# Kernel tuning notes

Hardware: AMD Instinct MI355X
Metric: run time of the kernel (lower is better)

## Reference

```python
import jax, jax.numpy as jnp
import numpy as np

B, N, C, H = 8, 4096, 768, 8


def setup_inputs() -> dict:
    key = jax.random.key(0)
    k1, k2, k3 = jax.random.split(key, 3)
    x = jax.random.normal(k1, (B, N, C), dtype=jnp.float32)
    W_qkv = jax.random.normal(k2, (C, 3 * C), dtype=jnp.float32) * 0.02
    W_proj = jax.random.normal(k3, (C, C), dtype=jnp.float32) * 0.02
    b_proj = jnp.zeros((C,), dtype=jnp.float32)
    temp = jnp.ones((H, 1, 1), dtype=jnp.float32)
    return {"x": x, "W_qkv": W_qkv, "W_proj": W_proj, "b_proj": b_proj, "temp": temp}


def reference(x, W_qkv, W_proj, b_proj, temp):
    b, n, c = x.shape
    h = temp.shape[0]
    d = c // h
    # qkv: [B,N,3C] -> [B,N,H,D,3]  (matches tf.reshape split order)
    qkv = (x @ W_qkv).reshape(b, n, h, d, 3)
    q, k, v = qkv[..., 0], qkv[..., 1], qkv[..., 2]
    # L2-normalize along the patch axis (axis=1), as tf.linalg.normalize
    q = q / jnp.linalg.norm(q, axis=1, keepdims=True)
    k = k / jnp.linalg.norm(k, axis=1, keepdims=True)
    # channel-wise (cross-covariance) attention: [B,H,D,D]
    attn = jnp.einsum('bnhd,bnhe->bhde', q, k) * temp
    attn = jax.nn.softmax(attn, axis=-1)
    # apply to v and fold heads back: [B,N,C]
    y = jnp.einsum('bhde,bnhe->bnhd', attn, v).reshape(b, n, c)
    return y @ W_proj + b_proj
```

## Files before the change

kernel.cpp:

```cpp
#include <hip/hip_runtime.h>

typedef __attribute__((ext_vector_type(8))) short short8;
typedef __attribute__((ext_vector_type(4))) float f32x4;

__device__ inline unsigned short f2b(float f) {
  unsigned int u = __builtin_bit_cast(unsigned int, f);
  u = (u + 0x7FFFu + ((u >> 16) & 1u)) >> 16;
  return (unsigned short)u;
}
__device__ inline float b2f(unsigned short s) {
  unsigned int u = ((unsigned int)s) << 16;
  return __builtin_bit_cast(float, u);
}

__device__ inline void async16(const void* g, void* l) {
  __builtin_amdgcn_global_load_lds((__attribute__((address_space(1))) void*)(g),
                                   (__attribute__((address_space(3))) void*)(l), 16, 0, 0);
}

__global__ void cvt_x(const float4* __restrict__ x, ushort4* __restrict__ xb, int n4) {
  int i = blockIdx.x * blockDim.x + threadIdx.x;
  int stride = gridDim.x * blockDim.x;
  for (; i < n4; i += stride) {
    float4 v = x[i];
    ushort4 o;
    o.x = f2b(v.x); o.y = f2b(v.y); o.z = f2b(v.z); o.w = f2b(v.w);
    xb[i] = o;
  }
}

__global__ __launch_bounds__(256) void t_wqkv(const float* __restrict__ W, unsigned short* __restrict__ Wt) {
  __shared__ float tile[32][33];
  int j0 = blockIdx.x * 32, c0 = blockIdx.y * 32;
  int tx = threadIdx.x & 31, ty = threadIdx.x >> 5;
#pragma unroll
  for (int r = 0; r < 32; r += 8)
    tile[ty + r][tx] = W[(size_t)(c0 + ty + r) * 2304 + j0 + tx];
  __syncthreads();
#pragma unroll
  for (int r = 0; r < 32; r += 8) {
    int j = j0 + ty + r;
    int h = j / 288, rem = j - h * 288;
    int d = rem / 3, s = rem - d * 3;
    int jj = s * 768 + h * 96 + d;
    Wt[(size_t)jj * 768 + c0 + tx] = f2b(tile[tx][ty + r]);
  }
}

__global__ __launch_bounds__(256) void t_wproj(const float* __restrict__ W, unsigned short* __restrict__ Wt) {
  __shared__ float tile[32][33];
  int j0 = blockIdx.x * 32, c0 = blockIdx.y * 32;
  int tx = threadIdx.x & 31, ty = threadIdx.x >> 5;
#pragma unroll
  for (int r = 0; r < 32; r += 8)
    tile[ty + r][tx] = W[(size_t)(c0 + ty + r) * 768 + j0 + tx];
  __syncthreads();
#pragma unroll
  for (int r = 0; r < 32; r += 8)
    Wt[(size_t)(j0 + ty + r) * 768 + c0 + tx] = f2b(tile[tx][ty + r]);
}

__global__ __launch_bounds__(512, 2) void gemm_qkv(
    const unsigned short* __restrict__ A, const unsigned short* __restrict__ Bt,
    unsigned short* __restrict__ Q, unsigned short* __restrict__ Kd, unsigned short* __restrict__ V) {
  extern __shared__ __align__(16) unsigned short smem[];
  const int tid = threadIdx.x;
  const int wave = tid >> 6, lane = tid & 63;
  const int mlane = lane & 15, quad = lane >> 4;
  const int m0 = blockIdx.x * 256, n0 = blockIdx.y * 256;
  const int ah = wave >> 2;
  const int wm = ah * 128;
  const int wn = (wave & 3) * 64;
  const int bh = wn >> 7;
  const int bl = wn & 64;

  f32x4 acc[8][4] = {};

  auto stage = [&](int kt, int c) {
    const int k0 = kt * 64;
#pragma unroll
    for (int h = 0; h < 4; ++h) {
      const unsigned short* src = (h < 2) ? A : Bt;
      const int rbase = ((h < 2) ? m0 : n0) + (h & 1) * 128;
      unsigned short* ldsbase = smem + c * 32768 + h * 8192;
#pragma unroll
      for (int i = 0; i < 2; ++i) {
        int ebase = i * 512 + (wave << 6);
        int e = ebase + lane;
        int row = e >> 3;
        int slot = (e & 7) ^ (row & 7);
        async16(src + (size_t)(rbase + row) * 768 + k0 + slot * 8, ldsbase + ebase * 8);
      }
    }
  };

  auto rdA = [&](const unsigned short* base, int mh, int kk, int f) -> short8 {
    int r = mh * 64 + f * 16 + mlane;
    return *(const short8*)&base[r * 64 + ((kk * 32 + quad * 8) ^ ((r & 7) << 3))];
  };
  auto rdB = [&](const unsigned short* base, int kk, int j) -> short8 {
    int r = bl + j * 16 + mlane;
    return *(const short8*)&base[r * 64 + ((kk * 32 + quad * 8) ^ ((r & 7) << 3))];
  };

  stage(0, 0);
  stage(1, 1);
  asm volatile("s_waitcnt vmcnt(8)" ::: "memory");
  __builtin_amdgcn_sched_barrier(0);
  __builtin_amdgcn_s_barrier();

#pragma unroll 1
  for (int t = 0; t < 12; ++t) {
    const int c = t & 1;
    const unsigned short* Abase = smem + c * 32768 + ah * 8192;
    const unsigned short* Bbase = smem + c * 32768 + 16384 + bh * 8192;
    short8 a0[4], a1[4], b0[4], b1[4];

#pragma unroll
    for (int j = 0; j < 4; ++j) b0[j] = rdB(Bbase, 0, j);
#pragma unroll
    for (int f = 0; f < 4; ++f) a0[f] = rdA(Abase, 0, 0, f);
    asm volatile("s_waitcnt lgkmcnt(0)" ::: "memory");
    __builtin_amdgcn_sched_barrier(0);
    __builtin_amdgcn_s_setprio(1);
#pragma unroll
    for (int f = 0; f < 4; ++f)
#pragma unroll
      for (int j = 0; j < 4; ++j)
        acc[f][j] = __builtin_amdgcn_mfma_f32_16x16x32_bf16(a0[f], b0[j], acc[f][j], 0, 0, 0);
    __builtin_amdgcn_s_setprio(0);
    __builtin_amdgcn_s_barrier();

#pragma unroll
    for (int f = 0; f < 4; ++f) a1[f] = rdA(Abase, 1, 0, f);
#pragma unroll
    for (int j = 0; j < 4; ++j) b1[j] = rdB(Bbase, 1, j);
    asm volatile("s_waitcnt lgkmcnt(0)" ::: "memory");
    __builtin_amdgcn_sched_barrier(0);
    __builtin_amdgcn_s_setprio(1);
#pragma unroll
    for (int f = 0; f < 4; ++f)
#pragma unroll
      for (int j = 0; j < 4; ++j)
        acc[4 + f][j] = __builtin_amdgcn_mfma_f32_16x16x32_bf16(a1[f], b0[j], acc[4 + f][j], 0, 0, 0);
    __builtin_amdgcn_s_setprio(0);
    __builtin_amdgcn_s_barrier();

#pragma unroll
    for (int f = 0; f < 4; ++f) a0[f] = rdA(Abase, 0, 1, f);
#pragma unroll
    for (int f = 0; f < 4; ++f) a1[f] = rdA(Abase, 1, 1, f);
    asm volatile("s_waitcnt lgkmcnt(0)" ::: "memory");
    __builtin_amdgcn_sched_barrier(0);
    __builtin_amdgcn_s_setprio(1);
#pragma unroll
    for (int f = 0; f < 4; ++f)
#pragma unroll
      for (int j = 0; j < 4; ++j)
        acc[f][j] = __builtin_amdgcn_mfma_f32_16x16x32_bf16(a0[f], b1[j], acc[f][j], 0, 0, 0);
    __builtin_amdgcn_s_setprio(0);
    __builtin_amdgcn_s_barrier();

    if (t < 10) stage(t + 2, c);
    __builtin_amdgcn_s_setprio(1);
#pragma unroll
    for (int f = 0; f < 4; ++f)
#pragma unroll
      for (int j = 0; j < 4; ++j)
        acc[4 + f][j] = __builtin_amdgcn_mfma_f32_16x16x32_bf16(a1[f], b1[j], acc[4 + f][j], 0, 0, 0);
    __builtin_amdgcn_s_setprio(0);
    if (t < 10) {
      asm volatile("s_waitcnt vmcnt(8)" ::: "memory");
      __builtin_amdgcn_sched_barrier(0);
      __builtin_amdgcn_s_barrier();
    } else if (t == 10) {
      asm volatile("s_waitcnt vmcnt(0)" ::: "memory");
      __builtin_amdgcn_sched_barrier(0);
      __builtin_amdgcn_s_barrier();
    }
  }

  const int bb = m0 >> 12;
  const int nbase = (m0 & 4095) + wm + quad * 4;
  unsigned short* dstp[4];
  size_t cb[4];
#pragma unroll
  for (int j = 0; j < 4; ++j) {
    int jj = n0 + wn + j * 16 + mlane;
    int s = (jj >= 1536) ? 2 : (jj >= 768) ? 1 : 0;
    int hd = jj - s * 768;
    int h = hd / 96;
    int d = hd - h * 96;
    dstp[j] = (s == 0) ? Q : (s == 1) ? Kd : V;
    cb[j] = ((size_t)(bb * 8 + h) * 4096) * 96 + d;
  }
#pragma unroll
  for (int mf = 0; mf < 8; ++mf) {
    int n = nbase + (mf >> 2) * 64 + (mf & 3) * 16;
#pragma unroll
    for (int r = 0; r < 4; ++r) {
#pragma unroll
      for (int j = 0; j < 4; ++j)
        dstp[j][cb[j] + (size_t)(n + r) * 96] = f2b(acc[mf][j][r]);
    }
  }
}

__global__ __launch_bounds__(256) void attn_partial(
    const unsigned short* __restrict__ Q, const unsigned short* __restrict__ Kd,
    float* __restrict__ Spart, float* __restrict__ sq, float* __restrict__ sk) {
  int chunk = blockIdx.x;
  int bh = blockIdx.y;
  __shared__ __align__(16) unsigned short QT[96 * 72];
  __shared__ __align__(16) unsigned short KT[96 * 72];
  int t = threadIdx.x;
  int wave = t >> 6, lane = t & 63, mlane = lane & 15, quad = lane >> 4;
  int wrow = (wave >> 1) * 48, wcol = (wave & 1) * 48;
  f32x4 acc[3][3] = {};
  const unsigned int* qp = (const unsigned int*)(Q + (size_t)bh * 4096 * 96);
  const unsigned int* kp = (const unsigned int*)(Kd + (size_t)bh * 4096 * 96);
  int c = t % 48, rg = t / 48;
  int nbeg = chunk * 256;
  float aq0 = 0.f, aq1 = 0.f, ak0 = 0.f, ak1 = 0.f;
  for (int n0 = nbeg; n0 < nbeg + 256; n0 += 64) {
    __syncthreads();
    if (rg < 5) {
      for (int n = rg; n < 64; n += 5) {
        unsigned int qv = qp[(size_t)(n0 + n) * 48 + c];
        unsigned int kv = kp[(size_t)(n0 + n) * 48 + c];
        QT[(2 * c) * 72 + n] = (unsigned short)(qv & 0xffff);
        QT[(2 * c + 1) * 72 + n] = (unsigned short)(qv >> 16);
        KT[(2 * c) * 72 + n] = (unsigned short)(kv & 0xffff);
        KT[(2 * c + 1) * 72 + n] = (unsigned short)(kv >> 16);
        float q0 = b2f((unsigned short)(qv & 0xffff)), q1 = b2f((unsigned short)(qv >> 16));
        float k0 = b2f((unsigned short)(kv & 0xffff)), k1 = b2f((unsigned short)(kv >> 16));
        aq0 += q0 * q0; aq1 += q1 * q1; ak0 += k0 * k0; ak1 += k1 * k1;
      }
    }
    __syncthreads();
#pragma unroll
    for (int kk = 0; kk < 64; kk += 32) {
      short8 a[3], bf[3];
#pragma unroll
      for (int f = 0; f < 3; ++f)
        a[f] = *(const short8*)&QT[(wrow + f * 16 + mlane) * 72 + kk + quad * 8];
#pragma unroll
      for (int f = 0; f < 3; ++f)
        bf[f] = *(const short8*)&KT[(wcol + f * 16 + mlane) * 72 + kk + quad * 8];
#pragma unroll
      for (int i = 0; i < 3; ++i)
#pragma unroll
        for (int j = 0; j < 3; ++j)
          acc[i][j] = __builtin_amdgcn_mfma_f32_16x16x32_bf16(a[i], bf[j], acc[i][j], 0, 0, 0);
    }
  }
  if (rg < 5) {
    atomicAdd(&sq[bh * 96 + 2 * c], aq0);
    atomicAdd(&sq[bh * 96 + 2 * c + 1], aq1);
    atomicAdd(&sk[bh * 96 + 2 * c], ak0);
    atomicAdd(&sk[bh * 96 + 2 * c + 1], ak1);
  }
  float* dst = Spart + ((size_t)bh * 16 + chunk) * 9216;
#pragma unroll
  for (int i = 0; i < 3; ++i)
#pragma unroll
    for (int j = 0; j < 3; ++j)
#pragma unroll
      for (int r = 0; r < 4; ++r)
        dst[(wrow + i * 16 + quad * 4 + r) * 96 + wcol + j * 16 + mlane] = acc[i][j][r];
}

__global__ __launch_bounds__(256) void attn_finalize(
    const float* __restrict__ Spart, const float* __restrict__ sq,
    const float* __restrict__ sk, const float* __restrict__ temp,
    unsigned short* __restrict__ Pt) {
  int bh = blockIdx.x, h = bh & 7;
  __shared__ float S[9216];
  __shared__ float rk[96], rq[96];
  int t = threadIdx.x;
  const float* base = Spart + (size_t)bh * 16 * 9216;
  if (t < 96) {
    rk[t] = rsqrtf(sk[bh * 96 + t]);
    rq[t] = rsqrtf(sq[bh * 96 + t]) * temp[h];
  }
  __syncthreads();
  for (int i = t; i < 9216; i += 256) {
    float s = 0.f;
#pragma unroll
    for (int c2 = 0; c2 < 16; ++c2) s += base[(size_t)c2 * 9216 + i];
    int d = i / 96, e = i - d * 96;
    S[i] = s * rq[d] * rk[e];
  }
  __syncthreads();
  if (t < 96) {
    int d = t;
    float mx = -1e30f;
    for (int e = 0; e < 96; ++e) mx = fmaxf(mx, S[d * 96 + e]);
    float sum = 0.f;
    for (int e = 0; e < 96; ++e) {
      float v = expf(S[d * 96 + e] - mx);
      S[d * 96 + e] = v;
      sum += v;
    }
    float inv = 1.0f / sum;
    for (int e = 0; e < 96; ++e)
      Pt[(size_t)bh * 9216 + e * 96 + d] = f2b(S[d * 96 + e] * inv);
  }
}

__global__ __launch_bounds__(256) void m_pre(
    const unsigned short* __restrict__ Wtp, const unsigned short* __restrict__ Pt,
    unsigned short* __restrict__ Mt) {
  int bh = blockIdx.y;
  int b = bh >> 3, h = bh & 7;
  int m0 = blockIdx.x * 128;
  int t = threadIdx.x, wave = t >> 6, lane = t & 63, mlane = lane & 15, quad = lane >> 4;
  const unsigned short* Pb = Pt + (size_t)bh * 9216;
  f32x4 acc[2][6] = {};
#pragma unroll
  for (int kk = 0; kk < 96; kk += 32) {
    short8 a[2], bfr[6];
#pragma unroll
    for (int i = 0; i < 2; ++i)
      a[i] = *(const short8*)&Wtp[(size_t)(m0 + wave * 32 + i * 16 + mlane) * 768 + h * 96 + kk + quad * 8];
#pragma unroll
    for (int j = 0; j < 6; ++j)
      bfr[j] = *(const short8*)&Pb[(j * 16 + mlane) * 96 + kk + quad * 8];
#pragma unroll
    for (int i = 0; i < 2; ++i)
#pragma unroll
      for (int j = 0; j < 6; ++j)
        acc[i][j] = __builtin_amdgcn_mfma_f32_16x16x32_bf16(a[i], bfr[j], acc[i][j], 0, 0, 0);
  }
#pragma unroll
  for (int i = 0; i < 2; ++i) {
    int cp = m0 + wave * 32 + i * 16 + quad * 4;
#pragma unroll
    for (int j = 0; j < 6; ++j) {
      int e = j * 16 + mlane;
#pragma unroll
      for (int r = 0; r < 4; ++r)
        Mt[((size_t)b * 768 + cp + r) * 768 + h * 96 + e] = f2b(acc[i][j][r]);
    }
  }
}

__global__ __launch_bounds__(512, 2) void gemm_out(
    const unsigned short* __restrict__ V, const unsigned short* __restrict__ Mt,
    const float* __restrict__ bias, float* __restrict__ out) {
  extern __shared__ __align__(16) unsigned short smem[];
  const int tid = threadIdx.x;
  const int wave = tid >> 6, lane = tid & 63;
  const int mlane = lane & 15, quad = lane >> 4;
  const int m0 = blockIdx.x * 256, n0 = blockIdx.y * 256;
  const int bb = m0 >> 12;
  const int nloc0 = m0 & 4095;
  const int ah = wave >> 2;
  const int wm = ah * 128;
  const int wn = (wave & 3) * 64;
  const int bhf = wn >> 7;
  const int bl = wn & 64;

  f32x4 acc[8][4] = {};

  auto stage = [&](int kt, int c) {
#pragma unroll
    for (int h = 0; h < 4; ++h) {
      unsigned short* ldsbase = smem + c * 32768 + h * 8192;
#pragma unroll
      for (int i = 0; i < 2; ++i) {
        int ebase = i * 512 + (wave << 6);
        int e = ebase + lane;
        int row = e >> 3;
        int slot = (e & 7) ^ (row & 7);
        if (h < 2) {
          int kc = kt * 8 + slot;
          int hh = kc / 12;
          int e0 = (kc - hh * 12) * 8;
          int n = nloc0 + (h & 1) * 128 + row;
          async16(V + ((size_t)(bb * 8 + hh) * 4096 + n) * 96 + e0, ldsbase + ebase * 8);
        } else {
          int col = n0 + (h & 1) * 128 + row;
          async16(Mt + ((size_t)bb * 768 + col) * 768 + kt * 64 + slot * 8, ldsbase + ebase * 8);
        }
      }
    }
  };

  auto rdA = [&](const unsigned short* base, int mh, int kk, int f) -> short8 {
    int r = mh * 64 + f * 16 + mlane;
    return *(const short8*)&base[r * 64 + ((kk * 32 + quad * 8) ^ ((r & 7) << 3))];
  };
  auto rdB = [&](const unsigned short* base, int kk, int j) -> short8 {
    int r = bl + j * 16 + mlane;
    return *(const short8*)&base[r * 64 + ((kk * 32 + quad * 8) ^ ((r & 7) << 3))];
  };

  stage(0, 0);
  stage(1, 1);
  asm volatile("s_waitcnt vmcnt(8)" ::: "memory");
  __builtin_amdgcn_sched_barrier(0);
  __builtin_amdgcn_s_barrier();

#pragma unroll 1
  for (int t = 0; t < 12; ++t) {
    const int c = t & 1;
    const unsigned short* Abase = smem + c * 32768 + ah * 8192;
    const unsigned short* Bbase = smem + c * 32768 + 16384 + bhf * 8192;
    short8 a0[4], a1[4], b0[4], b1[4];

#pragma unroll
    for (int j = 0; j < 4; ++j) b0[j] = rdB(Bbase, 0, j);
#pragma unroll
    for (int f = 0; f < 4; ++f) a0[f] = rdA(Abase, 0, 0, f);
    asm volatile("s_waitcnt lgkmcnt(0)" ::: "memory");
    __builtin_amdgcn_sched_barrier(0);
    __builtin_amdgcn_s_setprio(1);
#pragma unroll
    for (int f = 0; f < 4; ++f)
#pragma unroll
      for (int j = 0; j < 4; ++j)
        acc[f][j] = __builtin_amdgcn_mfma_f32_16x16x32_bf16(a0[f], b0[j], acc[f][j], 0, 0, 0);
    __builtin_amdgcn_s_setprio(0);
    __builtin_amdgcn_s_barrier();

#pragma unroll
    for (int f = 0; f < 4; ++f) a1[f] = rdA(Abase, 1, 0, f);
#pragma unroll
    for (int j = 0; j < 4; ++j) b1[j] = rdB(Bbase, 1, j);
    asm volatile("s_waitcnt lgkmcnt(0)" ::: "memory");
    __builtin_amdgcn_sched_barrier(0);
    __builtin_amdgcn_s_setprio(1);
#pragma unroll
    for (int f = 0; f < 4; ++f)
#pragma unroll
      for (int j = 0; j < 4; ++j)
        acc[4 + f][j] = __builtin_amdgcn_mfma_f32_16x16x32_bf16(a1[f], b0[j], acc[4 + f][j], 0, 0, 0);
    __builtin_amdgcn_s_setprio(0);
    __builtin_amdgcn_s_barrier();

#pragma unroll
    for (int f = 0; f < 4; ++f) a0[f] = rdA(Abase, 0, 1, f);
#pragma unroll
    for (int f = 0; f < 4; ++f) a1[f] = rdA(Abase, 1, 1, f);
    asm volatile("s_waitcnt lgkmcnt(0)" ::: "memory");
    __builtin_amdgcn_sched_barrier(0);
    __builtin_amdgcn_s_setprio(1);
#pragma unroll
    for (int f = 0; f < 4; ++f)
#pragma unroll
      for (int j = 0; j < 4; ++j)
        acc[f][j] = __builtin_amdgcn_mfma_f32_16x16x32_bf16(a0[f], b1[j], acc[f][j], 0, 0, 0);
    __builtin_amdgcn_s_setprio(0);
    __builtin_amdgcn_s_barrier();

    if (t < 10) stage(t + 2, c);
    __builtin_amdgcn_s_setprio(1);
#pragma unroll
    for (int f = 0; f < 4; ++f)
#pragma unroll
      for (int j = 0; j < 4; ++j)
        acc[4 + f][j] = __builtin_amdgcn_mfma_f32_16x16x32_bf16(a1[f], b1[j], acc[4 + f][j], 0, 0, 0);
    __builtin_amdgcn_s_setprio(0);
    if (t < 10) {
      asm volatile("s_waitcnt vmcnt(8)" ::: "memory");
      __builtin_amdgcn_sched_barrier(0);
      __builtin_amdgcn_s_barrier();
    } else if (t == 10) {
      asm volatile("s_waitcnt vmcnt(0)" ::: "memory");
      __builtin_amdgcn_sched_barrier(0);
      __builtin_amdgcn_s_barrier();
    }
  }

#pragma unroll
  for (int j = 0; j < 4; ++j) {
    int col = n0 + wn + j * 16 + mlane;
    float bv = bias[col];
#pragma unroll
    for (int mf = 0; mf < 8; ++mf) {
      int m = m0 + wm + (mf >> 2) * 64 + (mf & 3) * 16 + quad * 4;
#pragma unroll
      for (int r = 0; r < 4; ++r)
        out[(size_t)(m + r) * 768 + col] = acc[mf][j][r] + bv;
    }
  }
}

extern "C" void kernel_launch(void* const* d_in, const int* in_sizes, int n_in,
                              void* d_out, int out_size, void* d_ws, size_t ws_size,
                              hipStream_t stream) {
  const float* x = (const float*)d_in[0];
  const float* Wqkv = (const float*)d_in[1];
  const float* Wproj = (const float*)d_in[2];
  const float* bias = (const float*)d_in[3];
  const float* temp = (const float*)d_in[4];
  float* out = (float*)d_out;

  char* ws = (char*)d_ws;
  size_t off = 0;
  auto alloc = [&](size_t bytes) -> void* {
    void* p = ws + off;
    off += (bytes + 255) & ~(size_t)255;
    return p;
  };
  unsigned short* xb = (unsigned short*)alloc(32768ull * 768 * 2);
  unsigned short* Wtq = (unsigned short*)alloc(2304ull * 768 * 2);
  unsigned short* Wtp = (unsigned short*)alloc(768ull * 768 * 2);
  unsigned short* Q = (unsigned short*)alloc(64ull * 4096 * 96 * 2);
  unsigned short* Kd = (unsigned short*)alloc(64ull * 4096 * 96 * 2);
  unsigned short* V = (unsigned short*)alloc(64ull * 4096 * 96 * 2);
  float* sq = (float*)alloc(64 * 96 * 4);
  float* sk = (float*)alloc(64 * 96 * 4);
  unsigned short* Pt = (unsigned short*)alloc(64ull * 9216 * 2);
  (void)off; (void)ws_size; (void)in_sizes; (void)n_in; (void)out_size;

  unsigned short* Mt = xb;

  float* Spart = out;

  static bool attr_set = false;
  if (!attr_set) {
    hipFuncSetAttribute((const void*)gemm_qkv, hipFuncAttributeMaxDynamicSharedMemorySize, 131072);
    hipFuncSetAttribute((const void*)gemm_out, hipFuncAttributeMaxDynamicSharedMemorySize, 131072);
    attr_set = true;
  }

  cvt_x<<<4096, 256, 0, stream>>>((const float4*)x, (ushort4*)xb, 32768 * 768 / 4);
  t_wqkv<<<dim3(72, 24), 256, 0, stream>>>(Wqkv, Wtq);
  t_wproj<<<dim3(24, 24), 256, 0, stream>>>(Wproj, Wtp);
  hipMemsetAsync(sq, 0, 64 * 96 * 4, stream);
  hipMemsetAsync(sk, 0, 64 * 96 * 4, stream);
  gemm_qkv<<<dim3(128, 9), 512, 131072, stream>>>(xb, Wtq, Q, Kd, V);
  attn_partial<<<dim3(16, 64), 256, 0, stream>>>(Q, Kd, Spart, sq, sk);
  attn_finalize<<<64, 256, 0, stream>>>(Spart, sq, sk, temp, Pt);
  m_pre<<<dim3(6, 64), 256, 0, stream>>>(Wtp, Pt, Mt);
  gemm_out<<<dim3(128, 3), 512, 131072, stream>>>(V, Mt, bias, out);
}
```

Baseline: 473.1 us.

## Store Q/K transposed from QKV GEMM and fuse norm sums into epilogue

The QKV GEMM epilogue now writes Q and K in a [bh][d][n] transposed layout with 8-byte vector stores, and computes the per-channel sum of squares there with wave shuffles and atomics. The attention-partial kernel then drops its LDS transpose staging and its norm accumulation, and loads MFMA operands straight from global memory with register double-buffering. This removes the scalar, bank-conflicting LDS transpose pass and the extra reads of Q and K. The cost is more atomics in the GEMM epilogue. Norms are now computed from fp32 accumulators rather than the bf16-rounded values.

```diff
diff --git a/kernel.cpp b/kernel.cpp
--- a/kernel.cpp
+++ b/kernel.cpp
@@ -62,7 +62,8 @@
 
 __global__ __launch_bounds__(512, 2) void gemm_qkv(
     const unsigned short* __restrict__ A, const unsigned short* __restrict__ Bt,
-    unsigned short* __restrict__ Q, unsigned short* __restrict__ Kd, unsigned short* __restrict__ V) {
+    unsigned short* __restrict__ Qt, unsigned short* __restrict__ Kt, unsigned short* __restrict__ V,
+    float* __restrict__ sq, float* __restrict__ sk) {
   extern __shared__ __align__(16) unsigned short smem[];
   const int tid = threadIdx.x;
   const int wave = tid >> 6, lane = tid & 63;
@@ -181,84 +182,90 @@
   }
 
   const int bb = m0 >> 12;
-  const int nbase = (m0 & 4095) + wm + quad * 4;
-  unsigned short* dstp[4];
-  size_t cb[4];
-#pragma unroll
-  for (int j = 0; j < 4; ++j) {
-    int jj = n0 + wn + j * 16 + mlane;
-    int s = (jj >= 1536) ? 2 : (jj >= 768) ? 1 : 0;
-    int hd = jj - s * 768;
-    int h = hd / 96;
-    int d = hd - h * 96;
-    dstp[j] = (s == 0) ? Q : (s == 1) ? Kd : V;
-    cb[j] = ((size_t)(bb * 8 + h) * 4096) * 96 + d;
-  }
-#pragma unroll
-  for (int mf = 0; mf < 8; ++mf) {
-    int n = nbase + (mf >> 2) * 64 + (mf & 3) * 16;
-#pragma unroll
-    for (int r = 0; r < 4; ++r) {
-#pragma unroll
-      for (int j = 0; j < 4; ++j)
-        dstp[j][cb[j] + (size_t)(n + r) * 96] = f2b(acc[mf][j][r]);
+  const int s = n0 / 768;
+  if (s < 2) {
+    unsigned short* dst = (s == 0) ? Qt : Kt;
+    float* ss = (s == 0) ? sq : sk;
+    const int n0s = n0 - s * 768;
+    const int mloc = (m0 & 4095) + wm;
+#pragma unroll
+    for (int j = 0; j < 4; ++j) {
+      int hd = n0s + wn + j * 16 + mlane;
+      int h = hd / 96, d = hd - h * 96;
+      size_t rowbase = ((size_t)(bb * 8 + h) * 96 + d) * 4096 + mloc;
+      float ssq = 0.f;
+#pragma unroll
+      for (int mf = 0; mf < 8; ++mf) {
+        int nl = (mf >> 2) * 64 + (mf & 3) * 16 + quad * 4;
+        ushort4 o;
+        o.x = f2b(acc[mf][j][0]); o.y = f2b(acc[mf][j][1]);
+        o.z = f2b(acc[mf][j][2]); o.w = f2b(acc[mf][j][3]);
+        *(ushort4*)(dst + rowbase + nl) = o;
+#pragma unroll
+        for (int r = 0; r < 4; ++r) ssq += acc[mf][j][r] * acc[mf][j][r];
+      }
+      ssq += __shfl_xor(ssq, 16);
+      ssq += __shfl_xor(ssq, 32);
+      if (quad == 0) atomicAdd(&ss[(bb * 8 + h) * 96 + d], ssq);
+    }
+  } else {
+    const int nbase = (m0 & 4095) + wm + quad * 4;
+    size_t cb[4];
+#pragma unroll
+    for (int j = 0; j < 4; ++j) {
+      int hd = n0 + wn + j * 16 + mlane - 1536;
+      int h = hd / 96;
+      int d = hd - h * 96;
+      cb[j] = ((size_t)(bb * 8 + h) * 4096) * 96 + d;
+    }
+#pragma unroll
+    for (int mf = 0; mf < 8; ++mf) {
+      int n = nbase + (mf >> 2) * 64 + (mf & 3) * 16;
+#pragma unroll
+      for (int r = 0; r < 4; ++r) {
+#pragma unroll
+        for (int j = 0; j < 4; ++j)
+          V[cb[j] + (size_t)(n + r) * 96] = f2b(acc[mf][j][r]);
+      }
     }
   }
 }
 
 __global__ __launch_bounds__(256) void attn_partial(
-    const unsigned short* __restrict__ Q, const unsigned short* __restrict__ Kd,
-    float* __restrict__ Spart, float* __restrict__ sq, float* __restrict__ sk) {
+    const unsigned short* __restrict__ Qt, const unsigned short* __restrict__ Kt,
+    float* __restrict__ Spart) {
   int chunk = blockIdx.x;
   int bh = blockIdx.y;
-  __shared__ __align__(16) unsigned short QT[96 * 72];
-  __shared__ __align__(16) unsigned short KT[96 * 72];
   int t = threadIdx.x;
   int wave = t >> 6, lane = t & 63, mlane = lane & 15, quad = lane >> 4;
   int wrow = (wave >> 1) * 48, wcol = (wave & 1) * 48;
+  const unsigned short* qp = Qt + (size_t)bh * 96 * 4096;
+  const unsigned short* kp = Kt + (size_t)bh * 96 * 4096;
   f32x4 acc[3][3] = {};
-  const unsigned int* qp = (const unsigned int*)(Q + (size_t)bh * 4096 * 96);
-  const unsigned int* kp = (const unsigned int*)(Kd + (size_t)bh * 4096 * 96);
-  int c = t % 48, rg = t / 48;
   int nbeg = chunk * 256;
-  float aq0 = 0.f, aq1 = 0.f, ak0 = 0.f, ak1 = 0.f;
-  for (int n0 = nbeg; n0 < nbeg + 256; n0 += 64) {
-    __syncthreads();
-    if (rg < 5) {
-      for (int n = rg; n < 64; n += 5) {
-        unsigned int qv = qp[(size_t)(n0 + n) * 48 + c];
-        unsigned int kv = kp[(size_t)(n0 + n) * 48 + c];
-        QT[(2 * c) * 72 + n] = (unsigned short)(qv & 0xffff);
-        QT[(2 * c + 1) * 72 + n] = (unsigned short)(qv >> 16);
-        KT[(2 * c) * 72 + n] = (unsigned short)(kv & 0xffff);
-        KT[(2 * c + 1) * 72 + n] = (unsigned short)(kv >> 16);
-        float q0 = b2f((unsigned short)(qv & 0xffff)), q1 = b2f((unsigned short)(qv >> 16));
-        float k0 = b2f((unsigned short)(kv & 0xffff)), k1 = b2f((unsigned short)(kv >> 16));
-        aq0 += q0 * q0; aq1 += q1 * q1; ak0 += k0 * k0; ak1 += k1 * k1;
+
+  short8 a[3], b[3], an[3], bn[3];
+#pragma unroll
+  for (int f = 0; f < 3; ++f) {
+    a[f] = *(const short8*)&qp[(size_t)(wrow + f * 16 + mlane) * 4096 + nbeg + quad * 8];
+    b[f] = *(const short8*)&kp[(size_t)(wcol + f * 16 + mlane) * 4096 + nbeg + quad * 8];
+  }
+#pragma unroll 1
+  for (int n0 = nbeg; n0 < nbeg + 256; n0 += 32) {
+    if (n0 + 32 < nbeg + 256) {
+#pragma unroll
+      for (int f = 0; f < 3; ++f) {
+        an[f] = *(const short8*)&qp[(size_t)(wrow + f * 16 + mlane) * 4096 + n0 + 32 + quad * 8];
+        bn[f] = *(const short8*)&kp[(size_t)(wcol + f * 16 + mlane) * 4096 + n0 + 32 + quad * 8];
       }
     }
-    __syncthreads();
-#pragma unroll
-    for (int kk = 0; kk < 64; kk += 32) {
-      short8 a[3], bf[3];
-#pragma unroll
-      for (int f = 0; f < 3; ++f)
-        a[f] = *(const short8*)&QT[(wrow + f * 16 + mlane) * 72 + kk + quad * 8];
-#pragma unroll
-      for (int f = 0; f < 3; ++f)
-        bf[f] = *(const short8*)&KT[(wcol + f * 16 + mlane) * 72 + kk + quad * 8];
-#pragma unroll
-      for (int i = 0; i < 3; ++i)
-#pragma unroll
-        for (int j = 0; j < 3; ++j)
-          acc[i][j] = __builtin_amdgcn_mfma_f32_16x16x32_bf16(a[i], bf[j], acc[i][j], 0, 0, 0);
-    }
-  }
-  if (rg < 5) {
-    atomicAdd(&sq[bh * 96 + 2 * c], aq0);
-    atomicAdd(&sq[bh * 96 + 2 * c + 1], aq1);
-    atomicAdd(&sk[bh * 96 + 2 * c], ak0);
-    atomicAdd(&sk[bh * 96 + 2 * c + 1], ak1);
+#pragma unroll
+    for (int i = 0; i < 3; ++i)
+#pragma unroll
+      for (int j = 0; j < 3; ++j)
+        acc[i][j] = __builtin_amdgcn_mfma_f32_16x16x32_bf16(a[i], b[j], acc[i][j], 0, 0, 0);
+#pragma unroll
+    for (int f = 0; f < 3; ++f) { a[f] = an[f]; b[f] = bn[f]; }
   }
   float* dst = Spart + ((size_t)bh * 16 + chunk) * 9216;
 #pragma unroll
@@ -507,8 +514,8 @@
   unsigned short* xb = (unsigned short*)alloc(32768ull * 768 * 2);
   unsigned short* Wtq = (unsigned short*)alloc(2304ull * 768 * 2);
   unsigned short* Wtp = (unsigned short*)alloc(768ull * 768 * 2);
-  unsigned short* Q = (unsigned short*)alloc(64ull * 4096 * 96 * 2);
-  unsigned short* Kd = (unsigned short*)alloc(64ull * 4096 * 96 * 2);
+  unsigned short* Qt = (unsigned short*)alloc(64ull * 96 * 4096 * 2);
+  unsigned short* Kt = (unsigned short*)alloc(64ull * 96 * 4096 * 2);
   unsigned short* V = (unsigned short*)alloc(64ull * 4096 * 96 * 2);
   float* sq = (float*)alloc(64 * 96 * 4);
   float* sk = (float*)alloc(64 * 96 * 4);
@@ -516,7 +523,6 @@
   (void)off; (void)ws_size; (void)in_sizes; (void)n_in; (void)out_size;
 
   unsigned short* Mt = xb;
-
   float* Spart = out;
 
   static bool attr_set = false;
@@ -531,8 +537,8 @@
   t_wproj<<<dim3(24, 24), 256, 0, stream>>>(Wproj, Wtp);
   hipMemsetAsync(sq, 0, 64 * 96 * 4, stream);
   hipMemsetAsync(sk, 0, 64 * 96 * 4, stream);
-  gemm_qkv<<<dim3(128, 9), 512, 131072, stream>>>(xb, Wtq, Q, Kd, V);
-  attn_partial<<<dim3(16, 64), 256, 0, stream>>>(Q, Kd, Spart, sq, sk);
+  gemm_qkv<<<dim3(128, 9), 512, 131072, stream>>>(xb, Wtq, Qt, Kt, V, sq, sk);
+  attn_partial<<<dim3(16, 64), 256, 0, stream>>>(Qt, Kt, Spart);
   attn_finalize<<<64, 256, 0, stream>>>(Spart, sq, sk, temp, Pt);
   m_pre<<<dim3(6, 64), 256, 0, stream>>>(Wtp, Pt, Mt);
   gemm_out<<<dim3(128, 3), 512, 131072, stream>>>(V, Mt, bias, out);
```

Result: no change. 466.9 us (-1.3%).
